# Kernel optimization log

Measured on AMD Instinct MI355X. Metric: run time of the kernel, lower is better.

## Reference

```python
import jax, jax.numpy as jnp
import numpy as np

N_NODES = 50000
N_EDGES = 800000
F_IN = 16
HEADS = 4
CONV_DIMS = [(16, 16), (16, 32), (32, 32), (32, 32), (32, 32), (32, 64)]
LIN_DIMS = [(128, 256), (256, 64), (64, 16), (16, 1)]


def setup_inputs() -> dict:
    key = jax.random.key(0)
    ks = iter(jax.random.split(key, 64))
    inp = {}
    inp["x"] = jax.random.normal(next(ks), (N_NODES, F_IN), dtype=jnp.float32)
    inp["edge_index"] = jax.random.randint(next(ks), (2, N_EDGES), 0, N_NODES, dtype=jnp.int32)
    for i, (ci, co) in enumerate(CONV_DIMS, 1):
        inp[f"W{i}"] = jax.random.normal(next(ks), (ci, HEADS * co), dtype=jnp.float32) * (1.0 / np.sqrt(ci))
        inp[f"U{i}"] = jax.random.normal(next(ks), (ci, HEADS), dtype=jnp.float32) * (1.0 / np.sqrt(ci))
        inp[f"c{i}"] = jnp.zeros((HEADS,), jnp.float32)
        inp[f"b{i}"] = jnp.zeros((co,), jnp.float32)
    for i, d in zip((1, 2, 3), (32, 32, 64)):
        inp[f"g{i}"] = jnp.ones((d,), jnp.float32)
        inp[f"be{i}"] = jnp.zeros((d,), jnp.float32)
    for name, (ci, co) in zip(("1", "2", "3", "o"), LIN_DIMS):
        inp[f"lw{name}"] = jax.random.normal(next(ks), (ci, co), dtype=jnp.float32) * (1.0 / np.sqrt(ci))
        inp[f"lb{name}"] = jnp.zeros((co,), jnp.float32)
    return inp


def _feast(x, src, dst, W, U, c, b):
    # FeaStConv (PyG): q = softmax_h(U^T (x_j - x_i) + c); out_i = mean_j sum_h q_h * (W_h x_j) + b
    n = x.shape[0]
    out_ch = W.shape[1] // HEADS
    q = jax.nn.softmax((x[src] - x[dst]) @ U + c, axis=-1)            # [E, H]
    xw = (x @ W).reshape(n, HEADS, out_ch)                            # [N, H, O]
    msg = jnp.einsum('eho,eh->eo', xw[src], q)                        # [E, O]
    s = jax.ops.segment_sum(msg, dst, num_segments=n)
    cnt = jax.ops.segment_sum(jnp.ones((src.shape[0], 1), msg.dtype), dst, num_segments=n)
    return s / jnp.maximum(cnt, 1.0) + b


def _bn(x, g, b, eps=1e-5):
    # training-mode BatchNorm over the node dimension
    m = x.mean(0)
    v = x.var(0)
    return (x - m) * jax.lax.rsqrt(v + eps) * g + b


def _forward(x, edge_index, convs, bns, lins):
    # FeaStConv adds self-loops by default
    loops = jnp.arange(x.shape[0], dtype=edge_index.dtype)
    src = jnp.concatenate([edge_index[0], loops])
    dst = jnp.concatenate([edge_index[1], loops])
    h = jax.nn.relu(_feast(x, src, dst, *convs[0]))
    x1 = _bn(jax.nn.relu(_feast(h, src, dst, *convs[1])), *bns[0])
    x2 = jax.nn.relu(_feast(x1, src, dst, *convs[2]))
    x2 = _bn(jax.nn.relu(_feast(x2, src, dst, *convs[3])), *bns[1])
    x3 = jax.nn.relu(_feast(x2, src, dst, *convs[4]))
    x3 = _bn(jax.nn.relu(_feast(x3, src, dst, *convs[5])), *bns[2])
    z = jax.nn.relu(jnp.concatenate([x1, x2, x3], axis=1))            # [N, 128]
    (lw1, lb1), (lw2, lb2), (lw3, lb3), (lwo, lbo) = lins
    z = jax.nn.relu(z @ lw1 + lb1)
    z = jax.nn.relu(z @ lw2 + lb2)
    z = jax.nn.relu(z @ lw3 + lb3)
    return jax.nn.sigmoid(z @ lwo + lbo)                              # [N, 1]


def reference(x, edge_index, W1, U1, c1, b1, W2, U2, c2, b2, W3, U3, c3, b3, W4, U4, c4, b4, W5, U5, c5, b5, W6, U6, c6, b6, g1, be1, g2, be2, g3, be3, lw1, lb1, lw2, lb2, lw3, lb3, lwo, lbo):
    convs = [(W1, U1, c1, b1), (W2, U2, c2, b2), (W3, U3, c3, b3), (W4, U4, c4, b4), (W5, U5, c5, b5), (W6, U6, c6, b6)]
    bns = [(g1, be1), (g2, be2), (g3, be3)]
    lins = [(lw1, lb1), (lw2, lb2), (lw3, lb3), (lwo, lbo)]
    return _forward(x, edge_index, convs, bns, lins)
```

## Files before the change

kernel.cpp:

```cpp
#include <hip/hip_runtime.h>

constexpr int NN = 50000;
constexpr int NE = 800000;

typedef _Float16 h8 __attribute__((ext_vector_type(8)));
typedef _Float16 h4v __attribute__((ext_vector_type(4)));
typedef float f32x4 __attribute__((ext_vector_type(4)));

__global__ void hist_kernel(const int* __restrict__ dst, int* __restrict__ deg) {
    int e = blockIdx.x * blockDim.x + threadIdx.x;
    if (e < NE) atomicAdd(&deg[dst[e]], 1);
}

__global__ __launch_bounds__(1024) void scan_kernel(const int* __restrict__ deg,
                                                    int* __restrict__ row_ptr) {
    __shared__ int wsum[16];
    __shared__ int chunk_total;
    int tid = threadIdx.x, wid = tid >> 6, lane = tid & 63;
    int carry = 0;
    for (int base = 0; base < NN; base += 1024) {
        int i = base + tid;
        int v = (i < NN) ? deg[i] : 0;
        int x = v;
#pragma unroll
        for (int off = 1; off < 64; off <<= 1) {
            int y = __shfl_up(x, off, 64);
            if (lane >= off) x += y;
        }
        if (lane == 63) wsum[wid] = x;
        __syncthreads();
        if (wid == 0) {
            int wv = (lane < 16) ? wsum[lane] : 0;
#pragma unroll
            for (int off = 1; off < 16; off <<= 1) {
                int y = __shfl_up(wv, off, 64);
                if (lane >= off) wv += y;
            }
            if (lane < 16) wsum[lane] = wv;
            if (lane == 15) chunk_total = wv;
        }
        __syncthreads();
        int wprefix = (wid == 0) ? 0 : wsum[wid - 1];
        if (i < NN) row_ptr[i] = carry + wprefix + x - v;
        carry += chunk_total;
        __syncthreads();
    }
    if (tid == 0) row_ptr[NN] = carry;
}

__global__ void fill_kernel(const int* __restrict__ src, const int* __restrict__ dst,
                            const int* __restrict__ row_ptr, int* __restrict__ fillc,
                            int* __restrict__ col, int* __restrict__ dstc) {
    int e = blockIdx.x * blockDim.x + threadIdx.x;
    if (e < NE) {
        int d = dst[e];
        int p = atomicAdd(&fillc[d], 1);
        int k = row_ptr[d] + p;
        col[k] = src[e];
        dstc[k] = d;
    }
}

template <int CI>
__global__ __launch_bounds__(256) void prep_kernel(const float* __restrict__ x,
                                                   const float* __restrict__ U,
                                                   _Float16* __restrict__ xh,
                                                   float* __restrict__ t) {
    __shared__ float Us[CI * 4];
    for (int i = threadIdx.x; i < CI * 4; i += 256) Us[i] = U[i];
    __syncthreads();
    int n = blockIdx.x * 256 + threadIdx.x;
    if (n >= NN) return;
    float xr[CI];
    const float4* xv = reinterpret_cast<const float4*>(x + (size_t)n * CI);
#pragma unroll
    for (int q = 0; q < CI / 4; q++) {
        float4 v = xv[q];
        xr[4 * q + 0] = v.x; xr[4 * q + 1] = v.y; xr[4 * q + 2] = v.z; xr[4 * q + 3] = v.w;
    }
    h8* xo = reinterpret_cast<h8*>(xh + (size_t)n * CI);
#pragma unroll
    for (int q = 0; q < CI / 8; q++) {
        h8 hv;
#pragma unroll
        for (int u = 0; u < 8; u++) hv[u] = (_Float16)xr[8 * q + u];
        xo[q] = hv;
    }
    float a0 = 0.f, a1 = 0.f, a2 = 0.f, a3 = 0.f;
#pragma unroll
    for (int k = 0; k < CI; k++) {
        float xk = xr[k];
        a0 = fmaf(xk, Us[k * 4 + 0], a0); a1 = fmaf(xk, Us[k * 4 + 1], a1);
        a2 = fmaf(xk, Us[k * 4 + 2], a2); a3 = fmaf(xk, Us[k * 4 + 3], a3);
    }
    reinterpret_cast<float4*>(t)[n] = make_float4(a0, a1, a2, a3);
}

template <int CO>
__global__ __launch_bounds__(256) void tU_kernel(const _Float16* __restrict__ xh,
                                                 const float* __restrict__ U,
                                                 float* __restrict__ t) {
    __shared__ float Us[CO * 4];
    for (int i = threadIdx.x; i < CO * 4; i += 256) Us[i] = U[i];
    __syncthreads();
    int n = blockIdx.x * 256 + threadIdx.x;
    if (n >= NN) return;
    const h8* xp = reinterpret_cast<const h8*>(xh + (size_t)n * CO);
    float t0 = 0.f, t1 = 0.f, t2 = 0.f, t3 = 0.f;
#pragma unroll
    for (int q8 = 0; q8 < CO / 8; q8++) {
        h8 v = xp[q8];
#pragma unroll
        for (int u = 0; u < 8; u++) {
            float r = (float)v[u];
            const float* us = &Us[(q8 * 8 + u) * 4];
            t0 = fmaf(r, us[0], t0); t1 = fmaf(r, us[1], t1);
            t2 = fmaf(r, us[2], t2); t3 = fmaf(r, us[3], t3);
        }
    }
    reinterpret_cast<float4*>(t)[n] = make_float4(t0, t1, t2, t3);
}

__global__ __launch_bounds__(256) void edgeq_kernel(const int* __restrict__ col,
                                                    const int* __restrict__ dstc,
                                                    const float* __restrict__ t,
                                                    const float* __restrict__ cvec,
                                                    h4v* __restrict__ qbuf) {
    int k = blockIdx.x * 256 + threadIdx.x;
    if (k >= NE) return;
    int s = col[k], d = dstc[k];
    float4 ts = reinterpret_cast<const float4*>(t)[s];
    float4 td = reinterpret_cast<const float4*>(t)[d];
    float4 cv = *reinterpret_cast<const float4*>(cvec);
    float d0 = ts.x - td.x + cv.x, d1 = ts.y - td.y + cv.y;
    float d2 = ts.z - td.z + cv.z, d3 = ts.w - td.w + cv.w;
    float mm = fmaxf(fmaxf(d0, d1), fmaxf(d2, d3));
    float q0 = __expf(d0 - mm), q1 = __expf(d1 - mm);
    float q2 = __expf(d2 - mm), q3 = __expf(d3 - mm);
    float is = 1.f / (q0 + q1 + q2 + q3);
    h4v q;
    q[0] = (_Float16)(q0 * is); q[1] = (_Float16)(q1 * is);
    q[2] = (_Float16)(q2 * is); q[3] = (_Float16)(q3 * is);
    qbuf[k] = q;
}

template <int CI>
__global__ __launch_bounds__(256) void aggC_kernel(const _Float16* __restrict__ xh,
                                                   const h4v* __restrict__ qbuf,
                                                   const float* __restrict__ cvec,
                                                   const int* __restrict__ row_ptr,
                                                   const int* __restrict__ col,
                                                   _Float16* __restrict__ y) {
    constexpr int SLOTS = 64 / CI;
    int lane = threadIdx.x & 63;
    int n = blockIdx.x * 4 + (threadIdx.x >> 6);
    if (n >= NN) return;
    int ch = lane & (CI - 1);
    int slot = lane / CI;
    float4 cv = *reinterpret_cast<const float4*>(cvec);
    float a0 = 0.f, a1 = 0.f, a2 = 0.f, a3 = 0.f;
    if (slot == 0) {
        float m = fmaxf(fmaxf(cv.x, cv.y), fmaxf(cv.z, cv.w));
        float s0 = __expf(cv.x - m), s1 = __expf(cv.y - m),
              s2 = __expf(cv.z - m), s3 = __expf(cv.w - m);
        float sinv = 1.f / (s0 + s1 + s2 + s3);
        float xself = (float)xh[(size_t)n * CI + ch];
        a0 = s0 * sinv * xself; a1 = s1 * sinv * xself;
        a2 = s2 * sinv * xself; a3 = s3 * sinv * xself;
    }
    int beg = row_ptr[n], end = row_ptr[n + 1];
#pragma unroll 4
    for (int e = beg + slot; e < end; e += SLOTS) {
        int s = col[e];
        h4v q = qbuf[e];
        float xv = (float)xh[(size_t)s * CI + ch];
        a0 = fmaf((float)q[0], xv, a0); a1 = fmaf((float)q[1], xv, a1);
        a2 = fmaf((float)q[2], xv, a2); a3 = fmaf((float)q[3], xv, a3);
    }
#pragma unroll
    for (int off = 32; off >= CI; off >>= 1) {
        a0 += __shfl_xor(a0, off); a1 += __shfl_xor(a1, off);
        a2 += __shfl_xor(a2, off); a3 += __shfl_xor(a3, off);
    }
    if (slot == 0) {
        float sc = 1.f / (float)(end - beg + 1);
        _Float16* yo = y + (size_t)n * 4 * CI + ch;
        yo[0]      = (_Float16)(a0 * sc);
        yo[CI]     = (_Float16)(a1 * sc);
        yo[2 * CI] = (_Float16)(a2 * sc);
        yo[3 * CI] = (_Float16)(a3 * sc);
    }
}

template <int K, int CO, int COB, bool STACKED, bool OUT16>
__global__ __launch_bounds__(256) void mfma_dense_kernel(const _Float16* __restrict__ A,
                                                         const float* __restrict__ W,
                                                         const float* __restrict__ bias,
                                                         void* __restrict__ outp) {
    constexpr int KS = K / 16;
    constexpr int OT = COB / 16;
    constexpr int CIc = K / 4;
    __shared__ _Float16 Bf[OT * KS * 64 * 4];
    __shared__ float bS[COB];
    int o0 = blockIdx.y * COB;
    for (int idx = threadIdx.x; idx < OT * KS * 64; idx += 256) {
        int lane = idx & 63;
        int ks = (idx >> 6) % KS;
        int ot = idx / (64 * KS);
        int o = o0 + ot * 16 + (lane & 15);
        int kb = ks * 16 + (lane >> 4) * 4;
        h4v v;
#pragma unroll
        for (int j = 0; j < 4; j++) {
            int k = kb + j;
            float wv;
            if constexpr (STACKED) wv = W[(k % CIc) * (4 * CO) + (k / CIc) * CO + o];
            else                   wv = W[k * CO + o];
            v[j] = (_Float16)wv;
        }
        *reinterpret_cast<h4v*>(&Bf[idx * 4]) = v;
    }
    for (int i = threadIdx.x; i < COB; i += 256) bS[i] = bias[o0 + i];
    __syncthreads();
    int wid = threadIdx.x >> 6, lane = threadIdx.x & 63;
    int row_in = lane & 15;
    int kgrp = lane >> 4;
    for (int mt = blockIdx.x * 4 + wid; mt < NN / 16; mt += gridDim.x * 4) {
        int m0 = mt * 16;
        f32x4 acc[OT];
#pragma unroll
        for (int t = 0; t < OT; t++) acc[t] = {0.f, 0.f, 0.f, 0.f};
        const _Float16* Ab = A + (size_t)(m0 + row_in) * K + kgrp * 4;
#pragma unroll
        for (int ks = 0; ks < KS; ks++) {
            h4v af = *reinterpret_cast<const h4v*>(Ab + ks * 16);
#pragma unroll
            for (int t = 0; t < OT; t++) {
                h4v bf = *reinterpret_cast<const h4v*>(&Bf[((t * KS + ks) * 64 + lane) * 4]);
                acc[t] = __builtin_amdgcn_mfma_f32_16x16x16f16(af, bf, acc[t], 0, 0, 0);
            }
        }
        int orow0 = m0 + kgrp * 4;
#pragma unroll
        for (int t = 0; t < OT; t++) {
            int col = o0 + t * 16 + row_in;
            float b = bS[t * 16 + row_in];
#pragma unroll
            for (int i = 0; i < 4; i++) {
                float v = fmaxf(acc[t][i] + b, 0.f);
                if constexpr (OUT16)
                    ((_Float16*)outp)[(size_t)(orow0 + i) * CO + col] = (_Float16)v;
                else
                    ((float*)outp)[(size_t)(orow0 + i) * CO + col] = v;
            }
        }
    }
}

template <int C>
__global__ __launch_bounds__(256) void bn_reduce_kernel(const float* __restrict__ a,
                                                        float* __restrict__ stats) {
    constexpr int R = 256 / C;
    int cidx = threadIdx.x % C;
    int r = threadIdx.x / C;
    float s = 0.f, s2 = 0.f;
    for (int n = blockIdx.x * R + r; n < NN; n += gridDim.x * R) {
        float v = a[(size_t)n * C + cidx];
        s += v; s2 = fmaf(v, v, s2);
    }
    __shared__ float ls[256], ls2[256];
    ls[threadIdx.x] = s; ls2[threadIdx.x] = s2;
    __syncthreads();
    for (int off = 128; off >= C; off >>= 1) {
        if (threadIdx.x < off) {
            ls[threadIdx.x] += ls[threadIdx.x + off];
            ls2[threadIdx.x] += ls2[threadIdx.x + off];
        }
        __syncthreads();
    }
    if (threadIdx.x < C) {
        atomicAdd(&stats[cidx], ls[threadIdx.x]);
        atomicAdd(&stats[C + cidx], ls2[threadIdx.x]);
    }
}

template <int C>
__global__ __launch_bounds__(256) void bn_norm_prep_kernel(const float* __restrict__ a,
                                                           const float* __restrict__ stats,
                                                           const float* __restrict__ g,
                                                           const float* __restrict__ be,
                                                           const float* __restrict__ U,
                                                           _Float16* __restrict__ xh,
                                                           float* __restrict__ t,
                                                           _Float16* __restrict__ zh,
                                                           int zoff) {
    __shared__ float mS[C], sS[C], beS[C], Us[C * 4];
    if (threadIdx.x < C) {
        int c = threadIdx.x;
        float mean = stats[c] * (1.f / NN);
        float var = stats[C + c] * (1.f / NN) - mean * mean;
        mS[c] = mean;
        sS[c] = rsqrtf(fmaxf(var, 0.f) + 1e-5f) * g[c];
        beS[c] = be[c];
    }
    for (int i = threadIdx.x; i < C * 4; i += 256) Us[i] = U[i];
    __syncthreads();
    int n = blockIdx.x * 256 + threadIdx.x;
    if (n >= NN) return;
    const float4* ap = reinterpret_cast<const float4*>(a + (size_t)n * C);
    h8* xo = reinterpret_cast<h8*>(xh + (size_t)n * C);
    h8* zo = reinterpret_cast<h8*>(zh + (size_t)n * 128 + zoff);
    float t0 = 0.f, t1 = 0.f, t2 = 0.f, t3 = 0.f;
#pragma unroll
    for (int q8 = 0; q8 < C / 8; q8++) {
        h8 hv, zv;
#pragma unroll
        for (int q4 = 0; q4 < 2; q4++) {
            int c4 = q8 * 2 + q4;
            float4 v = ap[c4];
            float r0 = (v.x - mS[c4 * 4 + 0]) * sS[c4 * 4 + 0] + beS[c4 * 4 + 0];
            float r1 = (v.y - mS[c4 * 4 + 1]) * sS[c4 * 4 + 1] + beS[c4 * 4 + 1];
            float r2 = (v.z - mS[c4 * 4 + 2]) * sS[c4 * 4 + 2] + beS[c4 * 4 + 2];
            float r3 = (v.w - mS[c4 * 4 + 3]) * sS[c4 * 4 + 3] + beS[c4 * 4 + 3];
            hv[q4 * 4 + 0] = (_Float16)r0; hv[q4 * 4 + 1] = (_Float16)r1;
            hv[q4 * 4 + 2] = (_Float16)r2; hv[q4 * 4 + 3] = (_Float16)r3;
            zv[q4 * 4 + 0] = (_Float16)fmaxf(r0, 0.f); zv[q4 * 4 + 1] = (_Float16)fmaxf(r1, 0.f);
            zv[q4 * 4 + 2] = (_Float16)fmaxf(r2, 0.f); zv[q4 * 4 + 3] = (_Float16)fmaxf(r3, 0.f);
            const float* us;
            us = &Us[(c4 * 4 + 0) * 4];
            t0 = fmaf(r0, us[0], t0); t1 = fmaf(r0, us[1], t1); t2 = fmaf(r0, us[2], t2); t3 = fmaf(r0, us[3], t3);
            us = &Us[(c4 * 4 + 1) * 4];
            t0 = fmaf(r1, us[0], t0); t1 = fmaf(r1, us[1], t1); t2 = fmaf(r1, us[2], t2); t3 = fmaf(r1, us[3], t3);
            us = &Us[(c4 * 4 + 2) * 4];
            t0 = fmaf(r2, us[0], t0); t1 = fmaf(r2, us[1], t1); t2 = fmaf(r2, us[2], t2); t3 = fmaf(r2, us[3], t3);
            us = &Us[(c4 * 4 + 3) * 4];
            t0 = fmaf(r3, us[0], t0); t1 = fmaf(r3, us[1], t1); t2 = fmaf(r3, us[2], t2); t3 = fmaf(r3, us[3], t3);
        }
        xo[q8] = hv;
        zo[q8] = zv;
    }
    reinterpret_cast<float4*>(t)[n] = make_float4(t0, t1, t2, t3);
}

template <int C>
__global__ __launch_bounds__(256) void bn_norm_z_kernel(const float* __restrict__ a,
                                                        const float* __restrict__ stats,
                                                        const float* __restrict__ g,
                                                        const float* __restrict__ be,
                                                        _Float16* __restrict__ zh,
                                                        int zoff) {
    __shared__ float mS[C], sS[C], beS[C];
    if (threadIdx.x < C) {
        int c = threadIdx.x;
        float mean = stats[c] * (1.f / NN);
        float var = stats[C + c] * (1.f / NN) - mean * mean;
        mS[c] = mean;
        sS[c] = rsqrtf(fmaxf(var, 0.f) + 1e-5f) * g[c];
        beS[c] = be[c];
    }
    __syncthreads();
    int n = blockIdx.x * 256 + threadIdx.x;
    if (n >= NN) return;
    const float4* ap = reinterpret_cast<const float4*>(a + (size_t)n * C);
    h8* zo = reinterpret_cast<h8*>(zh + (size_t)n * 128 + zoff);
#pragma unroll
    for (int q8 = 0; q8 < C / 8; q8++) {
        h8 zv;
#pragma unroll
        for (int q4 = 0; q4 < 2; q4++) {
            int c4 = q8 * 2 + q4;
            float4 v = ap[c4];
            zv[q4 * 4 + 0] = (_Float16)fmaxf((v.x - mS[c4 * 4 + 0]) * sS[c4 * 4 + 0] + beS[c4 * 4 + 0], 0.f);
            zv[q4 * 4 + 1] = (_Float16)fmaxf((v.y - mS[c4 * 4 + 1]) * sS[c4 * 4 + 1] + beS[c4 * 4 + 1], 0.f);
            zv[q4 * 4 + 2] = (_Float16)fmaxf((v.z - mS[c4 * 4 + 2]) * sS[c4 * 4 + 2] + beS[c4 * 4 + 2], 0.f);
            zv[q4 * 4 + 3] = (_Float16)fmaxf((v.w - mS[c4 * 4 + 3]) * sS[c4 * 4 + 3] + beS[c4 * 4 + 3], 0.f);
        }
        zo[q8] = zv;
    }
}

__global__ __launch_bounds__(256) void lin3o_kernel(const _Float16* __restrict__ z2,
                                                    const float* __restrict__ lw3,
                                                    const float* __restrict__ lb3,
                                                    const float* __restrict__ lwo,
                                                    const float* __restrict__ lbo,
                                                    float* __restrict__ out) {
    __shared__ float W3s[64 * 16];
    __shared__ float Wos[16];
    __shared__ float b3s[16];
    for (int i = threadIdx.x; i < 64 * 16; i += 256) W3s[i] = lw3[i];
    if (threadIdx.x < 16) { Wos[threadIdx.x] = lwo[threadIdx.x]; b3s[threadIdx.x] = lb3[threadIdx.x]; }
    __syncthreads();
    int n = blockIdx.x * 256 + threadIdx.x;
    if (n >= NN) return;
    float acc[16];
#pragma unroll
    for (int u = 0; u < 16; u++) acc[u] = b3s[u];
    const h8* zp = reinterpret_cast<const h8*>(z2 + (size_t)n * 64);
#pragma unroll
    for (int k8 = 0; k8 < 8; k8++) {
        h8 v = zp[k8];
#pragma unroll
        for (int u = 0; u < 8; u++) {
            float vf = (float)v[u];
            const float* w = &W3s[(k8 * 8 + u) * 16];
#pragma unroll
            for (int o = 0; o < 16; o++) acc[o] = fmaf(vf, w[o], acc[o]);
        }
    }
    float s = lbo[0];
#pragma unroll
    for (int u = 0; u < 16; u++) s = fmaf(fmaxf(acc[u], 0.f), Wos[u], s);
    out[n] = 1.f / (1.f + __expf(-s));
}

extern "C" void kernel_launch(void* const* d_in, const int* in_sizes, int n_in,
                              void* d_out, int out_size, void* d_ws, size_t ws_size,
                              hipStream_t stream) {
    const float* x = (const float*)d_in[0];
    const int* ei = (const int*)d_in[1];
    const int* esrc = ei;
    const int* edst = ei + NE;
    const float* W[6]; const float* U[6]; const float* C[6]; const float* B[6];
    for (int i = 0; i < 6; i++) {
        W[i] = (const float*)d_in[2 + 4 * i];
        U[i] = (const float*)d_in[3 + 4 * i];
        C[i] = (const float*)d_in[4 + 4 * i];
        B[i] = (const float*)d_in[5 + 4 * i];
    }
    const float* g1 = (const float*)d_in[26]; const float* be1 = (const float*)d_in[27];
    const float* g2 = (const float*)d_in[28]; const float* be2 = (const float*)d_in[29];
    const float* g3 = (const float*)d_in[30]; const float* be3 = (const float*)d_in[31];
    const float* lw1 = (const float*)d_in[32]; const float* lb1 = (const float*)d_in[33];
    const float* lw2 = (const float*)d_in[34]; const float* lb2 = (const float*)d_in[35];
    const float* lw3 = (const float*)d_in[36]; const float* lb3 = (const float*)d_in[37];
    const float* lwo = (const float*)d_in[38]; const float* lbo = (const float*)d_in[39];

    char* w = (char*)d_ws;
    size_t o = 0;
    auto take = [&](size_t bytes) -> char* {
        char* p = w + o;
        o = (o + bytes + 255) & ~(size_t)255;
        return p;
    };
    int* deg = (int*)take((size_t)NN * 4);
    int* fillc = (int*)take((size_t)NN * 4);
    float* stats = (float*)take(3 * 256 * 4);
    size_t zero_bytes = o;
    int* row_ptr = (int*)take((size_t)(NN + 1) * 4);
    int* colA = (int*)take((size_t)NE * 4);
    int* dstc = (int*)take((size_t)NE * 4);
    h4v* qbuf = (h4v*)take((size_t)NE * 8);
    float* t = (float*)take((size_t)NN * 4 * 4);
    _Float16* xh = (_Float16*)take((size_t)NN * 32 * 2);
    char* A = take((size_t)NN * 256 * 2);
    _Float16* y = (_Float16*)A;
    _Float16* z1h = (_Float16*)A;
    _Float16* zh = (_Float16*)take((size_t)NN * 128 * 2);
    float* tmp = (float*)take((size_t)NN * 64 * 4);
    _Float16* z2h = (_Float16*)tmp;
    float* st0 = stats, *st1 = stats + 256, *st2 = stats + 512;

    hipMemsetAsync(d_ws, 0, zero_bytes, stream);

    const int EB = (NE + 255) / 256;
    const int NB = (NN + 255) / 256;
    const int GB = 250;

    hist_kernel<<<EB, 256, 0, stream>>>(edst, deg);
    scan_kernel<<<1, 1024, 0, stream>>>(deg, row_ptr);
    fill_kernel<<<EB, 256, 0, stream>>>(esrc, edst, row_ptr, fillc, colA, dstc);

    prep_kernel<16><<<NB, 256, 0, stream>>>(x, U[0], xh, t);
    edgeq_kernel<<<EB, 256, 0, stream>>>(colA, dstc, t, C[0], qbuf);
    aggC_kernel<16><<<NN / 4, 256, 0, stream>>>(xh, qbuf, C[0], row_ptr, colA, y);
    mfma_dense_kernel<64, 16, 16, true, true><<<dim3(GB, 1), 256, 0, stream>>>(y, W[0], B[0], xh);
    tU_kernel<16><<<NB, 256, 0, stream>>>(xh, U[1], t);
    edgeq_kernel<<<EB, 256, 0, stream>>>(colA, dstc, t, C[1], qbuf);
    aggC_kernel<16><<<NN / 4, 256, 0, stream>>>(xh, qbuf, C[1], row_ptr, colA, y);
    mfma_dense_kernel<64, 32, 32, true, false><<<dim3(GB, 1), 256, 0, stream>>>(y, W[1], B[1], tmp);
    bn_reduce_kernel<32><<<256, 256, 0, stream>>>(tmp, st0);
    bn_norm_prep_kernel<32><<<NB, 256, 0, stream>>>(tmp, st0, g1, be1, U[2], xh, t, zh, 0);
    edgeq_kernel<<<EB, 256, 0, stream>>>(colA, dstc, t, C[2], qbuf);
    aggC_kernel<32><<<NN / 4, 256, 0, stream>>>(xh, qbuf, C[2], row_ptr, colA, y);
    mfma_dense_kernel<128, 32, 32, true, true><<<dim3(GB, 1), 256, 0, stream>>>(y, W[2], B[2], xh);
    tU_kernel<32><<<NB, 256, 0, stream>>>(xh, U[3], t);
    edgeq_kernel<<<EB, 256, 0, stream>>>(colA, dstc, t, C[3], qbuf);
    aggC_kernel<32><<<NN / 4, 256, 0, stream>>>(xh, qbuf, C[3], row_ptr, colA, y);
    mfma_dense_kernel<128, 32, 32, true, false><<<dim3(GB, 1), 256, 0, stream>>>(y, W[3], B[3], tmp);
    bn_reduce_kernel<32><<<256, 256, 0, stream>>>(tmp, st1);
    bn_norm_prep_kernel<32><<<NB, 256, 0, stream>>>(tmp, st1, g2, be2, U[4], xh, t, zh, 32);
    edgeq_kernel<<<EB, 256, 0, stream>>>(colA, dstc, t, C[4], qbuf);
    aggC_kernel<32><<<NN / 4, 256, 0, stream>>>(xh, qbuf, C[4], row_ptr, colA, y);
    mfma_dense_kernel<128, 32, 32, true, true><<<dim3(GB, 1), 256, 0, stream>>>(y, W[4], B[4], xh);
    tU_kernel<32><<<NB, 256, 0, stream>>>(xh, U[5], t);
    edgeq_kernel<<<EB, 256, 0, stream>>>(colA, dstc, t, C[5], qbuf);
    aggC_kernel<32><<<NN / 4, 256, 0, stream>>>(xh, qbuf, C[5], row_ptr, colA, y);
    mfma_dense_kernel<128, 64, 64, true, false><<<dim3(GB, 1), 256, 0, stream>>>(y, W[5], B[5], tmp);
    bn_reduce_kernel<64><<<256, 256, 0, stream>>>(tmp, st2);
    bn_norm_z_kernel<64><<<NB, 256, 0, stream>>>(tmp, st2, g3, be3, zh, 64);

    mfma_dense_kernel<128, 256, 64, false, true><<<dim3(GB, 4), 256, 0, stream>>>(zh, lw1, lb1, z1h);
    mfma_dense_kernel<256, 64, 64, false, true><<<dim3(GB, 1), 256, 0, stream>>>(z1h, lw2, lb2, z2h);
    lin3o_kernel<<<NB, 256, 0, stream>>>(z2h, lw3, lb3, lwo, lbo, (float*)d_out);
}
```

Baseline: 652.8 us.

## Parallelize CSR scan, pack src/dst pairs, use two-wave aggregation per node

Replaces the single-block serial prefix scan with a three-kernel multi-block scan that also writes fill cursors, so fill no longer reads row_ptr. Source and destination indices are packed into one int2 array, so edge kernels issue a single 8-byte load instead of two separate loads. The aggregation kernel now gives each node 128 threads (two wavefronts) and combines their partial sums through shared memory. This spreads the neighbor gathers over more lanes, at the cost of a block barrier, extra launches, and aggC reading 8 bytes per edge where it used only the source index.

```diff
diff --git a/kernel.cpp b/kernel.cpp
--- a/kernel.cpp
+++ b/kernel.cpp
@@ -2,6 +2,7 @@
 
 constexpr int NN = 50000;
 constexpr int NE = 800000;
+constexpr int SNB = (NN + 255) / 256;
 
 typedef _Float16 h8 __attribute__((ext_vector_type(8)));
 typedef _Float16 h4v __attribute__((ext_vector_type(4)));
@@ -12,52 +13,68 @@
     if (e < NE) atomicAdd(&deg[dst[e]], 1);
 }
 
-__global__ __launch_bounds__(1024) void scan_kernel(const int* __restrict__ deg,
-                                                    int* __restrict__ row_ptr) {
-    __shared__ int wsum[16];
-    __shared__ int chunk_total;
-    int tid = threadIdx.x, wid = tid >> 6, lane = tid & 63;
-    int carry = 0;
-    for (int base = 0; base < NN; base += 1024) {
-        int i = base + tid;
-        int v = (i < NN) ? deg[i] : 0;
-        int x = v;
-#pragma unroll
-        for (int off = 1; off < 64; off <<= 1) {
-            int y = __shfl_up(x, off, 64);
-            if (lane >= off) x += y;
-        }
-        if (lane == 63) wsum[wid] = x;
-        __syncthreads();
-        if (wid == 0) {
-            int wv = (lane < 16) ? wsum[lane] : 0;
-#pragma unroll
-            for (int off = 1; off < 16; off <<= 1) {
-                int y = __shfl_up(wv, off, 64);
-                if (lane >= off) wv += y;
-            }
-            if (lane < 16) wsum[lane] = wv;
-            if (lane == 15) chunk_total = wv;
-        }
-        __syncthreads();
-        int wprefix = (wid == 0) ? 0 : wsum[wid - 1];
-        if (i < NN) row_ptr[i] = carry + wprefix + x - v;
-        carry += chunk_total;
-        __syncthreads();
-    }
-    if (tid == 0) row_ptr[NN] = carry;
+__global__ __launch_bounds__(256) void scan_bsum_kernel(const int* __restrict__ deg,
+                                                        int* __restrict__ bsum) {
+    int i = blockIdx.x * 256 + threadIdx.x;
+    int v = (i < NN) ? deg[i] : 0;
+#pragma unroll
+    for (int off = 32; off > 0; off >>= 1) v += __shfl_xor(v, off);
+    __shared__ int ws[4];
+    if ((threadIdx.x & 63) == 0) ws[threadIdx.x >> 6] = v;
+    __syncthreads();
+    if (threadIdx.x == 0) bsum[blockIdx.x] = ws[0] + ws[1] + ws[2] + ws[3];
+}
+
+__global__ __launch_bounds__(256) void scan_tops_kernel(const int* __restrict__ bsum,
+                                                        int* __restrict__ bpre) {
+    int tid = threadIdx.x;
+    int v = (tid < SNB) ? bsum[tid] : 0;
+    int lane = tid & 63, wid = tid >> 6;
+    int x = v;
+#pragma unroll
+    for (int off = 1; off < 64; off <<= 1) {
+        int y = __shfl_up(x, off, 64);
+        if (lane >= off) x += y;
+    }
+    __shared__ int wsum[4];
+    if (lane == 63) wsum[wid] = x;
+    __syncthreads();
+    int wpre = 0;
+    for (int w = 0; w < wid; w++) wpre += wsum[w];
+    if (tid < SNB) bpre[tid] = wpre + x - v;
+    if (tid == 0) bpre[SNB] = wsum[0] + wsum[1] + wsum[2] + wsum[3];
+}
+
+__global__ __launch_bounds__(256) void scan_final_kernel(const int* __restrict__ deg,
+                                                         const int* __restrict__ bpre,
+                                                         int* __restrict__ row_ptr,
+                                                         int* __restrict__ fillc) {
+    int i = blockIdx.x * 256 + threadIdx.x;
+    int v = (i < NN) ? deg[i] : 0;
+    int lane = threadIdx.x & 63, wid = threadIdx.x >> 6;
+    int x = v;
+#pragma unroll
+    for (int off = 1; off < 64; off <<= 1) {
+        int y = __shfl_up(x, off, 64);
+        if (lane >= off) x += y;
+    }
+    __shared__ int wsum[4];
+    if (lane == 63) wsum[wid] = x;
+    __syncthreads();
+    int wpre = 0;
+    for (int w = 0; w < wid; w++) wpre += wsum[w];
+    int ex = bpre[blockIdx.x] + wpre + x - v;
+    if (i < NN) { row_ptr[i] = ex; fillc[i] = ex; }
+    if (i == 0) row_ptr[NN] = bpre[SNB];
 }
 
 __global__ void fill_kernel(const int* __restrict__ src, const int* __restrict__ dst,
-                            const int* __restrict__ row_ptr, int* __restrict__ fillc,
-                            int* __restrict__ col, int* __restrict__ dstc) {
+                            int* __restrict__ fillc, int2* __restrict__ col2) {
     int e = blockIdx.x * blockDim.x + threadIdx.x;
     if (e < NE) {
         int d = dst[e];
-        int p = atomicAdd(&fillc[d], 1);
-        int k = row_ptr[d] + p;
-        col[k] = src[e];
-        dstc[k] = d;
+        int k = atomicAdd(&fillc[d], 1);
+        col2[k] = make_int2(src[e], d);
     }
 }
 
@@ -121,16 +138,15 @@
     reinterpret_cast<float4*>(t)[n] = make_float4(t0, t1, t2, t3);
 }
 
-__global__ __launch_bounds__(256) void edgeq_kernel(const int* __restrict__ col,
-                                                    const int* __restrict__ dstc,
+__global__ __launch_bounds__(256) void edgeq_kernel(const int2* __restrict__ col2,
                                                     const float* __restrict__ t,
                                                     const float* __restrict__ cvec,
                                                     h4v* __restrict__ qbuf) {
     int k = blockIdx.x * 256 + threadIdx.x;
     if (k >= NE) return;
-    int s = col[k], d = dstc[k];
-    float4 ts = reinterpret_cast<const float4*>(t)[s];
-    float4 td = reinterpret_cast<const float4*>(t)[d];
+    int2 sd = col2[k];
+    float4 ts = reinterpret_cast<const float4*>(t)[sd.x];
+    float4 td = reinterpret_cast<const float4*>(t)[sd.y];
     float4 cv = *reinterpret_cast<const float4*>(cvec);
     float d0 = ts.x - td.x + cv.x, d1 = ts.y - td.y + cv.y;
     float d2 = ts.z - td.z + cv.z, d3 = ts.w - td.w + cv.w;
@@ -149,14 +165,16 @@
                                                    const h4v* __restrict__ qbuf,
                                                    const float* __restrict__ cvec,
                                                    const int* __restrict__ row_ptr,
-                                                   const int* __restrict__ col,
+                                                   const int2* __restrict__ col2,
                                                    _Float16* __restrict__ y) {
-    constexpr int SLOTS = 64 / CI;
-    int lane = threadIdx.x & 63;
-    int n = blockIdx.x * 4 + (threadIdx.x >> 6);
-    if (n >= NN) return;
-    int ch = lane & (CI - 1);
-    int slot = lane / CI;
+    constexpr int SLOTS = 128 / CI;
+    __shared__ float part[2][CI * 4];
+    int tid = threadIdx.x;
+    int half = tid >> 7;
+    int lt = tid & 127;
+    int n = blockIdx.x * 2 + half;
+    int ch = lt & (CI - 1);
+    int slot = lt / CI;
     float4 cv = *reinterpret_cast<const float4*>(cvec);
     float a0 = 0.f, a1 = 0.f, a2 = 0.f, a3 = 0.f;
     if (slot == 0) {
@@ -169,9 +187,9 @@
         a2 = s2 * sinv * xself; a3 = s3 * sinv * xself;
     }
     int beg = row_ptr[n], end = row_ptr[n + 1];
-#pragma unroll 4
+#pragma unroll 2
     for (int e = beg + slot; e < end; e += SLOTS) {
-        int s = col[e];
+        int s = col2[e].x;
         h4v q = qbuf[e];
         float xv = (float)xh[(size_t)s * CI + ch];
         a0 = fmaf((float)q[0], xv, a0); a1 = fmaf((float)q[1], xv, a1);
@@ -182,7 +200,14 @@
         a0 += __shfl_xor(a0, off); a1 += __shfl_xor(a1, off);
         a2 += __shfl_xor(a2, off); a3 += __shfl_xor(a3, off);
     }
-    if (slot == 0) {
+    if (lt >= 64 && lt < 64 + CI) {
+        part[half][ch * 4 + 0] = a0; part[half][ch * 4 + 1] = a1;
+        part[half][ch * 4 + 2] = a2; part[half][ch * 4 + 3] = a3;
+    }
+    __syncthreads();
+    if (lt < CI) {
+        a0 += part[half][ch * 4 + 0]; a1 += part[half][ch * 4 + 1];
+        a2 += part[half][ch * 4 + 2]; a3 += part[half][ch * 4 + 3];
         float sc = 1.f / (float)(end - beg + 1);
         _Float16* yo = y + (size_t)n * 4 * CI + ch;
         yo[0]      = (_Float16)(a0 * sc);
@@ -444,12 +469,13 @@
         return p;
     };
     int* deg = (int*)take((size_t)NN * 4);
-    int* fillc = (int*)take((size_t)NN * 4);
     float* stats = (float*)take(3 * 256 * 4);
     size_t zero_bytes = o;
+    int* fillc = (int*)take((size_t)NN * 4);
     int* row_ptr = (int*)take((size_t)(NN + 1) * 4);
-    int* colA = (int*)take((size_t)NE * 4);
-    int* dstc = (int*)take((size_t)NE * 4);
+    int* bsum = (int*)take((size_t)(SNB + 1) * 4);
+    int* bpre = (int*)take((size_t)(SNB + 1) * 4);
+    int2* col2 = (int2*)take((size_t)NE * 8);
     h4v* qbuf = (h4v*)take((size_t)NE * 8);
     float* t = (float*)take((size_t)NN * 4 * 4);
     _Float16* xh = (_Float16*)take((size_t)NN * 32 * 2);
@@ -468,34 +494,36 @@
     const int GB = 250;
 
     hist_kernel<<<EB, 256, 0, stream>>>(edst, deg);
-    scan_kernel<<<1, 1024, 0, stream>>>(deg, row_ptr);
-    fill_kernel<<<EB, 256, 0, stream>>>(esrc, edst, row_ptr, fillc, colA, dstc);
+    scan_bsum_kernel<<<SNB, 256, 0, stream>>>(deg, bsum);
+    scan_tops_kernel<<<1, 256, 0, stream>>>(bsum, bpre);
+    scan_final_kernel<<<SNB, 256, 0, stream>>>(deg, bpre, row_ptr, fillc);
+    fill_kernel<<<EB, 256, 0, stream>>>(esrc, edst, fillc, col2);
 
     prep_kernel<16><<<NB, 256, 0, stream>>>(x, U[0], xh, t);
-    edgeq_kernel<<<EB, 256, 0, stream>>>(colA, dstc, t, C[0], qbuf);
-    aggC_kernel<16><<<NN / 4, 256, 0, stream>>>(xh, qbuf, C[0], row_ptr, colA, y);
+    edgeq_kernel<<<EB, 256, 0, stream>>>(col2, t, C[0], qbuf);
+    aggC_kernel<16><<<NN / 2, 256, 0, stream>>>(xh, qbuf, C[0], row_ptr, col2, y);
     mfma_dense_kernel<64, 16, 16, true, true><<<dim3(GB, 1), 256, 0, stream>>>(y, W[0], B[0], xh);
     tU_kernel<16><<<NB, 256, 0, stream>>>(xh, U[1], t);
-    edgeq_kernel<<<EB, 256, 0, stream>>>(colA, dstc, t, C[1], qbuf);
-    aggC_kernel<16><<<NN / 4, 256, 0, stream>>>(xh, qbuf, C[1], row_ptr, colA, y);
+    edgeq_kernel<<<EB, 256, 0, stream>>>(col2, t, C[1], qbuf);
+    aggC_kernel<16><<<NN / 2, 256, 0, stream>>>(xh, qbuf, C[1], row_ptr, col2, y);
     mfma_dense_kernel<64, 32, 32, true, false><<<dim3(GB, 1), 256, 0, stream>>>(y, W[1], B[1], tmp);
     bn_reduce_kernel<32><<<256, 256, 0, stream>>>(tmp, st0);
     bn_norm_prep_kernel<32><<<NB, 256, 0, stream>>>(tmp, st0, g1, be1, U[2], xh, t, zh, 0);
-    edgeq_kernel<<<EB, 256, 0, stream>>>(colA, dstc, t, C[2], qbuf);
-    aggC_kernel<32><<<NN / 4, 256, 0, stream>>>(xh, qbuf, C[2], row_ptr, colA, y);
+    edgeq_kernel<<<EB, 256, 0, stream>>>(col2, t, C[2], qbuf);
+    aggC_kernel<32><<<NN / 2, 256, 0, stream>>>(xh, qbuf, C[2], row_ptr, col2, y);
     mfma_dense_kernel<128, 32, 32, true, true><<<dim3(GB, 1), 256, 0, stream>>>(y, W[2], B[2], xh);
     tU_kernel<32><<<NB, 256, 0, stream>>>(xh, U[3], t);
-    edgeq_kernel<<<EB, 256, 0, stream>>>(colA, dstc, t, C[3], qbuf);
-    aggC_kernel<32><<<NN / 4, 256, 0, stream>>>(xh, qbuf, C[3], row_ptr, colA, y);
+    edgeq_kernel<<<EB, 256, 0, stream>>>(col2, t, C[3], qbuf);
+    aggC_kernel<32><<<NN / 2, 256, 0, stream>>>(xh, qbuf, C[3], row_ptr, col2, y);
     mfma_dense_kernel<128, 32, 32, true, false><<<dim3(GB, 1), 256, 0, stream>>>(y, W[3], B[3], tmp);
     bn_reduce_kernel<32><<<256, 256, 0, stream>>>(tmp, st1);
     bn_norm_prep_kernel<32><<<NB, 256, 0, stream>>>(tmp, st1, g2, be2, U[4], xh, t, zh, 32);
-    edgeq_kernel<<<EB, 256, 0, stream>>>(colA, dstc, t, C[4], qbuf);
-    aggC_kernel<32><<<NN / 4, 256, 0, stream>>>(xh, qbuf, C[4], row_ptr, colA, y);
+    edgeq_kernel<<<EB, 256, 0, stream>>>(col2, t, C[4], qbuf);
+    aggC_kernel<32><<<NN / 2, 256, 0, stream>>>(xh, qbuf, C[4], row_ptr, col2, y);
     mfma_dense_kernel<128, 32, 32, true, true><<<dim3(GB, 1), 256, 0, stream>>>(y, W[4], B[4], xh);
     tU_kernel<32><<<NB, 256, 0, stream>>>(xh, U[5], t);
-    edgeq_kernel<<<EB, 256, 0, stream>>>(colA, dstc, t, C[5], qbuf);
-    aggC_kernel<32><<<NN / 4, 256, 0, stream>>>(xh, qbuf, C[5], row_ptr, colA, y);
+    edgeq_kernel<<<EB, 256, 0, stream>>>(col2, t, C[5], qbuf);
+    aggC_kernel<32><<<NN / 2, 256, 0, stream>>>(xh, qbuf, C[5], row_ptr, col2, y);
     mfma_dense_kernel<128, 64, 64, true, false><<<dim3(GB, 1), 256, 0, stream>>>(y, W[5], B[5], tmp);
     bn_reduce_kernel<64><<<256, 256, 0, stream>>>(tmp, st2);
     bn_norm_z_kernel<64><<<NB, 256, 0, stream>>>(tmp, st2, g3, be3, zh, 64);
```

New measurement: 653.0 us. No clear change (+0.0%).
